# Kernel tuning notes

Measured on AMD Instinct MI355X. Metric: run time of the kernel, lower is better.

## Reference

```python
import jax, jax.numpy as jnp
from jax import lax
import numpy as np

EPS = 1e-5

def lc2d(x, w, b, stride):
    # x: [B,H,W]; w: [oh,ow,kh,kw] unshared kernels; b: [oh,ow]
    oh, ow, kh, kw = w.shape
    hi = jnp.arange(oh)[:, None] * stride + jnp.arange(kh)[None, :]  # [oh,kh]
    wi = jnp.arange(ow)[:, None] * stride + jnp.arange(kw)[None, :]  # [ow,kw]
    patches = x[:, hi[:, None, :, None], wi[None, :, None, :]]  # [B,oh,ow,kh,kw]
    return jnp.einsum('bhwkl,hwkl->bhw', patches, w) + b

def ln2d(x, g, b):
    # LayerNorm over last two dims (per-sample)
    m = jnp.mean(x, axis=(-2, -1), keepdims=True)
    v = jnp.var(x, axis=(-2, -1), keepdims=True)
    return (x - m) * lax.rsqrt(v + EPS) * g + b

def maxpool2(x):
    # MaxPool2d(kernel=2, stride=2) on [B,H,W]
    return lax.reduce_window(x, -jnp.inf, lax.max, (1, 2, 2), (1, 2, 2), 'VALID')

def setup_inputs() -> dict:
    key = jax.random.key(0)
    ks = iter(jax.random.split(key, 16))
    d = {'x': jax.random.normal(next(ks), (128, 224, 224), jnp.float32)}
    layer_specs = [(109, 7), (50, 5), (48, 3), (22, 3), (20, 3), (8, 3)]
    for i, (o, k) in enumerate(layer_specs, 1):
        std = float(np.sqrt(2.0 / (k + k)))  # xavier_normal_ on a [k,k] kernel
        d[f'w{i}'] = jax.random.normal(next(ks), (o, o, k, k), jnp.float32) * std
        d[f'b{i}'] = jnp.zeros((o, o), jnp.float32)
        d[f'g{i}'] = jnp.ones((o, o), jnp.float32)
        d[f'be{i}'] = jnp.zeros((o, o), jnp.float32)
    d['fcw'] = jax.random.normal(next(ks), (1000, 64), jnp.float32) * float(np.sqrt(1.0 / 64))
    d['fcb'] = jnp.zeros((1000,), jnp.float32)
    return d

def reference(x, w1, b1, g1, be1, w2, b2, g2, be2, w3, b3, g3, be3,
              w4, b4, g4, be4, w5, b5, g5, be5, w6, b6, g6, be6, fcw, fcb):
    # dropout is inference-mode identity (p=0)
    h = ln2d(jax.nn.relu(lc2d(x, w1, b1, 2)), g1, be1)   # [B,109,109]
    h = maxpool2(h)                                       # [B,54,54]
    h = ln2d(jax.nn.relu(lc2d(h, w2, b2, 1)), g2, be2)   # [B,50,50]
    h = ln2d(jax.nn.relu(lc2d(h, w3, b3, 1)), g3, be3)   # [B,48,48]
    h = maxpool2(h)                                       # [B,24,24]
    h = ln2d(jax.nn.relu(lc2d(h, w4, b4, 1)), g4, be4)   # [B,22,22]
    h = ln2d(jax.nn.relu(lc2d(h, w5, b5, 1)), g5, be5)   # [B,20,20]
    h = maxpool2(h)                                       # [B,10,10]
    h = ln2d(jax.nn.relu(lc2d(h, w6, b6, 1)), g6, be6)   # [B,8,8]
    logits = h.reshape(h.shape[0], -1) @ fcw.T + fcb      # [B,1000]
    return jax.nn.softmax(logits, axis=1)
```

## Files before the change

kernel.cpp:

```cpp
#include <hip/hip_runtime.h>
#include <math.h>

static constexpr float kEps = 1e-5f;

__global__ __launch_bounds__(256)
void transpose_w1(const float* __restrict__ w1, float* __restrict__ t1)
{
    const int tid = blockIdx.x * blockDim.x + threadIdx.x;
    const int nt  = gridDim.x * blockDim.x;
    for (int i = tid; i < 49 * 109 * 112; i += nt) {
        const int kk = i / (109 * 112), r = i % (109 * 112);
        const int oh = r / 112, ow = r % 112;
        t1[i] = (ow < 109) ? w1[(oh * 109 + ow) * 49 + kk] : 0.f;
    }
}

__global__ __launch_bounds__(128)
void conv1(const float* __restrict__ x, const float* __restrict__ wt,
           const float* __restrict__ bias, float* __restrict__ y,
           float* __restrict__ partial,
           const float* __restrict__ w2, const float* __restrict__ w3,
           const float* __restrict__ w4, const float* __restrict__ w5,
           const float* __restrict__ w6,
           const float* __restrict__ g1, const float* __restrict__ be1,
           float* __restrict__ w2t, float* __restrict__ w3t,
           float* __restrict__ w4t, float* __restrict__ w5t,
           float* __restrict__ w6t,
           float4* __restrict__ g1p, float4* __restrict__ be1p)
{
    constexpr int IN = 224, OUT = 109, K = 7, RPS = 4, QPR = 28, NS = 28;
    constexpr int ROWS = (RPS - 1) * 2 + K;
    __shared__ __align__(16) float xs0[ROWS * IN];
    __shared__ __align__(16) float xs1[ROWS * IN];
    __shared__ float red[2][4];

    const int s = blockIdx.x, bp = blockIdx.y, t = threadIdx.x;

    if (bp == 64) {
        const int tid = s * 128 + t;
        const int nt  = 28 * 128;
        for (int i = tid; i < 25 * 50 * 52; i += nt) {
            const int kk = i / (50 * 52), r = i % (50 * 52);
            const int oh = r / 52, ow = r % 52;
            w2t[i] = (ow < 50) ? w2[(oh * 50 + ow) * 25 + kk] : 0.f;
        }
        for (int i = tid; i < 9 * 2304; i += nt) {
            const int kk = i / 2304, idx = i % 2304;
            w3t[i] = w3[idx * 9 + kk];
        }
        for (int i = tid; i < 9 * 22 * 24; i += nt) {
            const int kk = i / (22 * 24), r = i % (22 * 24);
            const int oh = r / 24, ow = r % 24;
            w4t[i] = (ow < 22) ? w4[(oh * 22 + ow) * 9 + kk] : 0.f;
        }
        for (int i = tid; i < 9 * 400; i += nt) {
            const int kk = i / 400, idx = i % 400;
            w5t[i] = w5[idx * 9 + kk];
        }
        for (int i = tid; i < 9 * 64; i += nt) {
            const int kk = i / 64, idx = i % 64;
            w6t[i] = w6[idx * 9 + kk];
        }
        for (int i = tid; i < 54 * 54; i += nt) {
            const int ph = i / 54, pw = i - ph * 54;
            const int i00 = (2 * ph) * 109 + 2 * pw, i10 = i00 + 109;
            g1p[i]  = make_float4(g1[i00],  g1[i00 + 1],  g1[i10],  g1[i10 + 1]);
            be1p[i] = make_float4(be1[i00], be1[i00 + 1], be1[i10], be1[i10 + 1]);
        }
        return;
    }

    const int b0 = 2 * bp, b1 = b0 + 1;
    const int oh0 = s * RPS, ih0 = oh0 * 2;
    const int nrows = min(ROWS, IN - ih0);
    {
        const float4* g0 = (const float4*)(x + ((size_t)b0 * IN + ih0) * IN);
        const float4* g1r = (const float4*)(x + ((size_t)b1 * IN + ih0) * IN);
        float4* s0 = (float4*)xs0;
        float4* s1 = (float4*)xs1;
        const int n4 = nrows * (IN / 4);
        for (int i = t; i < n4; i += 128) { s0[i] = g0[i]; s1[i] = g1r[i]; }
    }
    __syncthreads();

    float lsum0 = 0.f, lsq0 = 0.f, lsum1 = 0.f, lsq1 = 0.f;
    if (t < RPS * QPR) {
        const int r = t / QPR, qc = t - r * QPR;
        const int oh = oh0 + r, ow0 = qc * 4;
        if (oh < OUT) {
            float acc0[4], acc1[4];
            #pragma unroll
            for (int o = 0; o < 4; ++o) {
                const float bv = (ow0 + o < OUT) ? bias[oh * OUT + ow0 + o] : 0.f;
                acc0[o] = bv; acc1[o] = bv;
            }
            const int lr0 = r * 2, c0 = ow0 * 2;
            #pragma unroll
            for (int kh = 0; kh < K; ++kh) {
                const float* p0 = xs0 + (lr0 + kh) * IN + c0;
                const float* p1 = xs1 + (lr0 + kh) * IN + c0;
                float a0[14], a1[14];
                #pragma unroll
                for (int i = 0; i < 7; ++i) {
                    const float2 v0 = *(const float2*)(p0 + 2 * i);
                    const float2 v1 = *(const float2*)(p1 + 2 * i);
                    a0[2 * i] = v0.x; a0[2 * i + 1] = v0.y;
                    a1[2 * i] = v1.x; a1[2 * i + 1] = v1.y;
                }
                #pragma unroll
                for (int kw = 0; kw < K; ++kw) {
                    const float4 w4 = *(const float4*)(wt + ((size_t)(kh * 7 + kw) * OUT + oh) * 112 + ow0);
                    acc0[0] = fmaf(a0[kw    ], w4.x, acc0[0]);  acc1[0] = fmaf(a1[kw    ], w4.x, acc1[0]);
                    acc0[1] = fmaf(a0[kw + 2], w4.y, acc0[1]);  acc1[1] = fmaf(a1[kw + 2], w4.y, acc1[1]);
                    acc0[2] = fmaf(a0[kw + 4], w4.z, acc0[2]);  acc1[2] = fmaf(a1[kw + 4], w4.z, acc1[2]);
                    acc0[3] = fmaf(a0[kw + 6], w4.w, acc0[3]);  acc1[3] = fmaf(a1[kw + 6], w4.w, acc1[3]);
                }
            }
            float4 st0, st1;
            #pragma unroll
            for (int o = 0; o < 4; ++o) {
                const float v0 = fmaxf(acc0[o], 0.f), v1 = fmaxf(acc1[o], 0.f);
                if (ow0 + o < OUT) {
                    lsum0 += v0; lsq0 = fmaf(v0, v0, lsq0);
                    lsum1 += v1; lsq1 = fmaf(v1, v1, lsq1);
                }
                (&st0.x)[o] = v0; (&st1.x)[o] = v1;
            }
            *(float4*)(y + ((size_t)b0 * OUT + oh) * 112 + ow0) = st0;
            *(float4*)(y + ((size_t)b1 * OUT + oh) * 112 + ow0) = st1;
        }
    }
    #pragma unroll
    for (int off = 32; off > 0; off >>= 1) {
        lsum0 += __shfl_down(lsum0, off, 64);  lsq0 += __shfl_down(lsq0, off, 64);
        lsum1 += __shfl_down(lsum1, off, 64);  lsq1 += __shfl_down(lsq1, off, 64);
    }
    if ((t & 63) == 0) {
        const int w = t >> 6;
        red[w][0] = lsum0; red[w][1] = lsq0; red[w][2] = lsum1; red[w][3] = lsq1;
    }
    __syncthreads();
    if (t == 0) {
        const float a = red[0][0] + red[1][0], bq = red[0][1] + red[1][1];
        const float c = red[0][2] + red[1][2], d  = red[0][3] + red[1][3];
        partial[((size_t)b0 * NS + s) * 2]     = a;
        partial[((size_t)b0 * NS + s) * 2 + 1] = bq;
        partial[((size_t)b1 * NS + s) * 2]     = c;
        partial[((size_t)b1 * NS + s) * 2 + 1] = d;
    }
}

__device__ inline float2 bstats(float ls, float lq, float invN, float (*red)[2], int t)
{
    #pragma unroll
    for (int off = 32; off > 0; off >>= 1) {
        ls += __shfl_down(ls, off, 64);
        lq += __shfl_down(lq, off, 64);
    }
    if ((t & 63) == 0) { red[t >> 6][0] = ls; red[t >> 6][1] = lq; }
    __syncthreads();
    float s = 0.f, q = 0.f;
    #pragma unroll
    for (int w = 0; w < 16; ++w) { s += red[w][0]; q += red[w][1]; }
    const float m = s * invN;
    return make_float2(m, rsqrtf(q * invN - m * m + kEps));
}

__global__ __launch_bounds__(1024)
void tail(const float* __restrict__ y1, const float* __restrict__ partial,
          const float4* __restrict__ g1p, const float4* __restrict__ be1p,
          const float* __restrict__ w2t, const float* __restrict__ b2,
          const float* __restrict__ g2, const float* __restrict__ be2,
          const float* __restrict__ w3t, const float* __restrict__ b3,
          const float* __restrict__ g3, const float* __restrict__ be3,
          const float* __restrict__ w4t, const float* __restrict__ b4,
          const float* __restrict__ g4, const float* __restrict__ be4,
          const float* __restrict__ w5t, const float* __restrict__ b5,
          const float* __restrict__ g5, const float* __restrict__ be5,
          const float* __restrict__ w6t, const float* __restrict__ b6,
          const float* __restrict__ g6, const float* __restrict__ be6,
          const float* __restrict__ fcw, const float* __restrict__ fcb,
          float* __restrict__ out)
{
    __shared__ __align__(16) float xs54[54 * 54 + 8];
    __shared__ __align__(16) float y50[50 * 52];
    __shared__ __align__(16) float y48[48 * 48];
    __shared__ __align__(16) float xs24[24 * 24 + 8];
    __shared__ __align__(16) float y22[22 * 24];
    __shared__ __align__(16) float y20[20 * 20];
    __shared__ __align__(16) float xs10[100];
    __shared__ float y8[64], h[64];
    __shared__ float red[16][2];

    const int b = blockIdx.x, t = threadIdx.x;
    const int lane = t & 63;

    float s = 0.f, q = 0.f;
    if (lane < 28) {
        const float2 p = *(const float2*)(partial + ((size_t)b * 28 + lane) * 2);
        s = p.x; q = p.y;
    }
    #pragma unroll
    for (int off = 32; off > 0; off >>= 1) {
        s += __shfl_down(s, off, 64);
        q += __shfl_down(q, off, 64);
    }
    s = __shfl(s, 0, 64); q = __shfl(q, 0, 64);
    const float m1 = s / 11881.f;
    const float r1 = rsqrtf(q / 11881.f - m1 * m1 + kEps);

    const float* yb = y1 + (size_t)b * 109 * 112;
    #pragma unroll
    for (int it = 0; it < 3; ++it) {
        const int idx = t + it * 1024;
        if (idx < 54 * 54) {
            const int ph = idx / 54, pw = idx - ph * 54;
            const int r0 = 2 * ph, c0 = 2 * pw;
            const float2 u0 = *(const float2*)(yb + r0 * 112 + c0);
            const float2 u1 = *(const float2*)(yb + (r0 + 1) * 112 + c0);
            const float4 g = g1p[idx], be = be1p[idx];
            const float v0 = (u0.x - m1) * r1 * g.x + be.x;
            const float v1 = (u0.y - m1) * r1 * g.y + be.y;
            const float v2 = (u1.x - m1) * r1 * g.z + be.z;
            const float v3 = (u1.y - m1) * r1 * g.w + be.w;
            xs54[ph * 54 + pw] = fmaxf(fmaxf(v0, v1), fmaxf(v2, v3));
        }
    }
    __syncthreads();

    float ls = 0.f, lq = 0.f;
    if (t < 650) {
        const int oh = t / 13, qc = t - oh * 13;
        const int ow0 = qc * 4;
        float acc[4];
        #pragma unroll
        for (int o = 0; o < 4; ++o) acc[o] = (ow0 + o < 50) ? b2[oh * 50 + ow0 + o] : 0.f;
        #pragma unroll
        for (int kh = 0; kh < 5; ++kh) {
            const float* xp = xs54 + (oh + kh) * 54 + ow0;
            float a[8];
            #pragma unroll
            for (int i = 0; i < 4; ++i) {
                const float2 v = *(const float2*)(xp + 2 * i);
                a[2 * i] = v.x; a[2 * i + 1] = v.y;
            }
            #pragma unroll
            for (int kw = 0; kw < 5; ++kw) {
                const float4 w4 = *(const float4*)(w2t + ((size_t)(kh * 5 + kw) * 50 + oh) * 52 + ow0);
                acc[0] = fmaf(a[kw    ], w4.x, acc[0]);
                acc[1] = fmaf(a[kw + 1], w4.y, acc[1]);
                acc[2] = fmaf(a[kw + 2], w4.z, acc[2]);
                acc[3] = fmaf(a[kw + 3], w4.w, acc[3]);
            }
        }
        #pragma unroll
        for (int o = 0; o < 4; ++o) {
            const float v = fmaxf(acc[o], 0.f);
            y50[oh * 52 + ow0 + o] = v;
            if (ow0 + o < 50) { ls += v; lq = fmaf(v, v, lq); }
        }
    }
    const float2 s2 = bstats(ls, lq, 1.f / 2500.f, red, t);

    #pragma unroll
    for (int it = 0; it < 3; ++it) {
        const int idx = t + it * 1024;
        if (idx < 2500) {
            const int oh = idx / 50, ow = idx - oh * 50;
            const int p = oh * 52 + ow;
            y50[p] = (y50[p] - s2.x) * s2.y * g2[idx] + be2[idx];
        }
    }
    __syncthreads();

    ls = 0.f; lq = 0.f;
    if (t < 576) {
        const int oh = t / 12, qc = t - oh * 12;
        const int ow0 = qc * 4;
        float acc[4];
        #pragma unroll
        for (int o = 0; o < 4; ++o) acc[o] = b3[oh * 48 + ow0 + o];
        #pragma unroll
        for (int kh = 0; kh < 3; ++kh) {
            const float* xp = y50 + (oh + kh) * 52 + ow0;
            float a[6];
            #pragma unroll
            for (int i = 0; i < 3; ++i) {
                const float2 v = *(const float2*)(xp + 2 * i);
                a[2 * i] = v.x; a[2 * i + 1] = v.y;
            }
            #pragma unroll
            for (int kw = 0; kw < 3; ++kw) {
                const float4 w4 = *(const float4*)(w3t + (size_t)(kh * 3 + kw) * 2304 + oh * 48 + ow0);
                acc[0] = fmaf(a[kw    ], w4.x, acc[0]);
                acc[1] = fmaf(a[kw + 1], w4.y, acc[1]);
                acc[2] = fmaf(a[kw + 2], w4.z, acc[2]);
                acc[3] = fmaf(a[kw + 3], w4.w, acc[3]);
            }
        }
        float4 st;
        #pragma unroll
        for (int o = 0; o < 4; ++o) {
            const float v = fmaxf(acc[o], 0.f);
            (&st.x)[o] = v; ls += v; lq = fmaf(v, v, lq);
        }
        *(float4*)(y48 + oh * 48 + ow0) = st;
    }
    const float2 s3 = bstats(ls, lq, 1.f / 2304.f, red, t);

    if (t < 576) {
        const int ph = t / 24, pw = t - ph * 24;
        const int r0 = 2 * ph, c0 = 2 * pw;
        const float2 u0 = *(const float2*)(y48 + r0 * 48 + c0);
        const float2 u1 = *(const float2*)(y48 + (r0 + 1) * 48 + c0);
        const int i00 = r0 * 48 + c0, i10 = i00 + 48;
        const float v0 = (u0.x - s3.x) * s3.y * g3[i00]     + be3[i00];
        const float v1 = (u0.y - s3.x) * s3.y * g3[i00 + 1] + be3[i00 + 1];
        const float v2 = (u1.x - s3.x) * s3.y * g3[i10]     + be3[i10];
        const float v3 = (u1.y - s3.x) * s3.y * g3[i10 + 1] + be3[i10 + 1];
        xs24[ph * 24 + pw] = fmaxf(fmaxf(v0, v1), fmaxf(v2, v3));
    }
    __syncthreads();

    ls = 0.f; lq = 0.f;
    if (t < 132) {
        const int oh = t / 6, qc = t - oh * 6;
        const int ow0 = qc * 4;
        float acc[4];
        #pragma unroll
        for (int o = 0; o < 4; ++o) acc[o] = (ow0 + o < 22) ? b4[oh * 22 + ow0 + o] : 0.f;
        #pragma unroll
        for (int kh = 0; kh < 3; ++kh) {
            const float* xp = xs24 + (oh + kh) * 24 + ow0;
            float a[6];
            #pragma unroll
            for (int i = 0; i < 3; ++i) {
                const float2 v = *(const float2*)(xp + 2 * i);
                a[2 * i] = v.x; a[2 * i + 1] = v.y;
            }
            #pragma unroll
            for (int kw = 0; kw < 3; ++kw) {
                const float4 w4 = *(const float4*)(w4t + ((size_t)(kh * 3 + kw) * 22 + oh) * 24 + ow0);
                acc[0] = fmaf(a[kw    ], w4.x, acc[0]);
                acc[1] = fmaf(a[kw + 1], w4.y, acc[1]);
                acc[2] = fmaf(a[kw + 2], w4.z, acc[2]);
                acc[3] = fmaf(a[kw + 3], w4.w, acc[3]);
            }
        }
        #pragma unroll
        for (int o = 0; o < 4; ++o) {
            const float v = fmaxf(acc[o], 0.f);
            y22[oh * 24 + ow0 + o] = v;
            if (ow0 + o < 22) { ls += v; lq = fmaf(v, v, lq); }
        }
    }
    const float2 s4 = bstats(ls, lq, 1.f / 484.f, red, t);

    if (t < 484) {
        const int oh = t / 22, ow = t - oh * 22;
        const int p = oh * 24 + ow;
        y22[p] = (y22[p] - s4.x) * s4.y * g4[t] + be4[t];
    }
    __syncthreads();

    ls = 0.f; lq = 0.f;
    if (t < 100) {
        const int oh = t / 5, qc = t - oh * 5;
        const int ow0 = qc * 4;
        float acc[4];
        #pragma unroll
        for (int o = 0; o < 4; ++o) acc[o] = b5[oh * 20 + ow0 + o];
        #pragma unroll
        for (int kh = 0; kh < 3; ++kh) {
            const float* xp = y22 + (oh + kh) * 24 + ow0;
            float a[6];
            #pragma unroll
            for (int i = 0; i < 3; ++i) {
                const float2 v = *(const float2*)(xp + 2 * i);
                a[2 * i] = v.x; a[2 * i + 1] = v.y;
            }
            #pragma unroll
            for (int kw = 0; kw < 3; ++kw) {
                const float4 w4 = *(const float4*)(w5t + (size_t)(kh * 3 + kw) * 400 + oh * 20 + ow0);
                acc[0] = fmaf(a[kw    ], w4.x, acc[0]);
                acc[1] = fmaf(a[kw + 1], w4.y, acc[1]);
                acc[2] = fmaf(a[kw + 2], w4.z, acc[2]);
                acc[3] = fmaf(a[kw + 3], w4.w, acc[3]);
            }
        }
        #pragma unroll
        for (int o = 0; o < 4; ++o) {
            const float v = fmaxf(acc[o], 0.f);
            y20[oh * 20 + ow0 + o] = v;
            ls += v; lq = fmaf(v, v, lq);
        }
    }
    const float2 s5 = bstats(ls, lq, 1.f / 400.f, red, t);

    if (t < 100) {
        const int ph = t / 10, pw = t - ph * 10;
        const int r0 = 2 * ph, c0 = 2 * pw;
        const float2 u0 = *(const float2*)(y20 + r0 * 20 + c0);
        const float2 u1 = *(const float2*)(y20 + (r0 + 1) * 20 + c0);
        const int i00 = r0 * 20 + c0, i10 = i00 + 20;
        const float v0 = (u0.x - s5.x) * s5.y * g5[i00]     + be5[i00];
        const float v1 = (u0.y - s5.x) * s5.y * g5[i00 + 1] + be5[i00 + 1];
        const float v2 = (u1.x - s5.x) * s5.y * g5[i10]     + be5[i10];
        const float v3 = (u1.y - s5.x) * s5.y * g5[i10 + 1] + be5[i10 + 1];
        xs10[ph * 10 + pw] = fmaxf(fmaxf(v0, v1), fmaxf(v2, v3));
    }
    __syncthreads();

    ls = 0.f; lq = 0.f;
    if (t < 16) {
        const int oh = t / 2, qc = t - oh * 2;
        const int ow0 = qc * 4;
        float acc[4];
        #pragma unroll
        for (int o = 0; o < 4; ++o) acc[o] = b6[oh * 8 + ow0 + o];
        #pragma unroll
        for (int kh = 0; kh < 3; ++kh) {
            const float* xp = xs10 + (oh + kh) * 10 + ow0;
            float a[6];
            #pragma unroll
            for (int i = 0; i < 3; ++i) {
                const float2 v = *(const float2*)(xp + 2 * i);
                a[2 * i] = v.x; a[2 * i + 1] = v.y;
            }
            #pragma unroll
            for (int kw = 0; kw < 3; ++kw) {
                const float4 w4 = *(const float4*)(w6t + (size_t)(kh * 3 + kw) * 64 + oh * 8 + ow0);
                acc[0] = fmaf(a[kw    ], w4.x, acc[0]);
                acc[1] = fmaf(a[kw + 1], w4.y, acc[1]);
                acc[2] = fmaf(a[kw + 2], w4.z, acc[2]);
                acc[3] = fmaf(a[kw + 3], w4.w, acc[3]);
            }
        }
        #pragma unroll
        for (int o = 0; o < 4; ++o) {
            const float v = fmaxf(acc[o], 0.f);
            y8[oh * 8 + ow0 + o] = v;
            ls += v; lq = fmaf(v, v, lq);
        }
    }
    const float2 s6 = bstats(ls, lq, 1.f / 64.f, red, t);

    if (t < 64) h[t] = (y8[t] - s6.x) * s6.y * g6[t] + be6[t];
    __syncthreads();

    float lj = -INFINITY;
    if (t < 1000) {
        const float4* wr = (const float4*)(fcw + (size_t)t * 64);
        float acc = fcb[t];
        #pragma unroll
        for (int k = 0; k < 16; ++k) {
            const float4 w4 = wr[k];
            acc = fmaf(h[4 * k], w4.x,
                  fmaf(h[4 * k + 1], w4.y,
                  fmaf(h[4 * k + 2], w4.z,
                  fmaf(h[4 * k + 3], w4.w, acc))));
        }
        lj = acc;
    }
    float mx = lj;
    #pragma unroll
    for (int off = 32; off > 0; off >>= 1) mx = fmaxf(mx, __shfl_down(mx, off, 64));
    if (lane == 0) red[t >> 6][0] = mx;
    __syncthreads();
    float gmax = red[0][0];
    #pragma unroll
    for (int w = 1; w < 16; ++w) gmax = fmaxf(gmax, red[w][0]);

    const float e = (t < 1000) ? __expf(lj - gmax) : 0.f;
    float ssum = e;
    #pragma unroll
    for (int off = 32; off > 0; off >>= 1) ssum += __shfl_down(ssum, off, 64);
    if (lane == 0) red[t >> 6][1] = ssum;
    __syncthreads();
    float tot = 0.f;
    #pragma unroll
    for (int w = 0; w < 16; ++w) tot += red[w][1];
    if (t < 1000) out[(size_t)b * 1000 + t] = e / tot;
}

extern "C" void kernel_launch(void* const* d_in, const int* in_sizes, int n_in,
                              void* d_out, int out_size, void* d_ws, size_t ws_size,
                              hipStream_t stream) {
    const float* x   = (const float*)d_in[0];
    const float* w1  = (const float*)d_in[1];
    const float* b1  = (const float*)d_in[2];
    const float* g1  = (const float*)d_in[3];
    const float* be1 = (const float*)d_in[4];
    const float* w2  = (const float*)d_in[5];
    const float* b2  = (const float*)d_in[6];
    const float* g2  = (const float*)d_in[7];
    const float* be2 = (const float*)d_in[8];
    const float* w3  = (const float*)d_in[9];
    const float* b3  = (const float*)d_in[10];
    const float* g3  = (const float*)d_in[11];
    const float* be3 = (const float*)d_in[12];
    const float* w4  = (const float*)d_in[13];
    const float* b4  = (const float*)d_in[14];
    const float* g4  = (const float*)d_in[15];
    const float* be4 = (const float*)d_in[16];
    const float* w5  = (const float*)d_in[17];
    const float* b5  = (const float*)d_in[18];
    const float* g5  = (const float*)d_in[19];
    const float* be5 = (const float*)d_in[20];
    const float* w6  = (const float*)d_in[21];
    const float* b6  = (const float*)d_in[22];
    const float* g6  = (const float*)d_in[23];
    const float* be6 = (const float*)d_in[24];
    const float* fcw = (const float*)d_in[25];
    const float* fcb = (const float*)d_in[26];

    float* y1p  = (float*)d_ws;
    float* w1t  = y1p  + 1562624;
    float* w2t  = w1t  + 598192;
    float* w3t  = w2t  + 65000;
    float* w4t  = w3t  + 20736;
    float* w5t  = w4t  + 4752;
    float* w6t  = w5t  + 3600;
    float* part = w6t  + 576;
    float* g1pp = part + 7168;
    float* be1pp= g1pp + 11664;

    transpose_w1<<<512, 256, 0, stream>>>(w1, w1t);

    conv1<<<dim3(28, 65), 128, 0, stream>>>(x, w1t, b1, y1p, part,
                                            w2, w3, w4, w5, w6, g1, be1,
                                            w2t, w3t, w4t, w5t, w6t,
                                            (float4*)g1pp, (float4*)be1pp);

    tail<<<128, 1024, 0, stream>>>(y1p, part,
                                   (const float4*)g1pp, (const float4*)be1pp,
                                   w2t, b2, g2, be2,
                                   w3t, b3, g3, be3,
                                   w4t, b4, g4, be4,
                                   w5t, b5, g5, be5,
                                   w6t, b6, g6, be6,
                                   fcw, fcb, (float*)d_out);
}
```

Before: 53.06 us.

## Restructure conv1 with strided column mapping, padded smem rows, larger row tiles

Conv1 now assigns each thread output columns qc, qc+28, qc+56 and qc+84 instead of four adjacent columns, and w1 is transposed into a matching interleaved layout so one float4 load still fetches all four weights. Shared-memory rows are padded to a 228-float stride to spread LDS bank accesses. Each block now covers 7 output rows with 256 threads instead of 4 rows with 128, so there are 16 row strips per sample instead of 28 and less halo is reloaded. In exchange the output stores become scalar instead of float4, and each thread makes more separate LDS reads.

After: 86.16 us. +62.4%, slower.

```diff
diff --git a/kernel.cpp b/kernel.cpp
--- a/kernel.cpp
+++ b/kernel.cpp
@@ -9,13 +9,16 @@
     const int tid = blockIdx.x * blockDim.x + threadIdx.x;
     const int nt  = gridDim.x * blockDim.x;
     for (int i = tid; i < 49 * 109 * 112; i += nt) {
-        const int kk = i / (109 * 112), r = i % (109 * 112);
-        const int oh = r / 112, ow = r % 112;
-        t1[i] = (ow < 109) ? w1[(oh * 109 + ow) * 49 + kk] : 0.f;
+        const int kk = i / 12208;
+        const int rem = i - kk * 12208;
+        const int oh = rem / 112, ow = rem - oh * 112;
+        const int qc = ow % 28, o = ow / 28;
+        const float v = (ow < 109) ? w1[(oh * 109 + ow) * 49 + kk] : 0.f;
+        t1[(((size_t)kk * 109 + oh) * 28 + qc) * 4 + o] = v;
     }
 }
 
-__global__ __launch_bounds__(128)
+__global__ __launch_bounds__(256)
 void conv1(const float* __restrict__ x, const float* __restrict__ wt,
            const float* __restrict__ bias, float* __restrict__ y,
            float* __restrict__ partial,
@@ -28,17 +31,18 @@
            float* __restrict__ w6t,
            float4* __restrict__ g1p, float4* __restrict__ be1p)
 {
-    constexpr int IN = 224, OUT = 109, K = 7, RPS = 4, QPR = 28, NS = 28;
-    constexpr int ROWS = (RPS - 1) * 2 + K;
-    __shared__ __align__(16) float xs0[ROWS * IN];
-    __shared__ __align__(16) float xs1[ROWS * IN];
-    __shared__ float red[2][4];
+    constexpr int IN = 224, OUT = 109, RPS = 7, NS = 16;
+    constexpr int ROWS = (RPS - 1) * 2 + 7;
+    constexpr int RSTR = 228;
+    __shared__ __align__(16) float xs0[ROWS * RSTR + 12];
+    __shared__ __align__(16) float xs1[ROWS * RSTR + 12];
+    __shared__ float red[4][4];
 
     const int s = blockIdx.x, bp = blockIdx.y, t = threadIdx.x;
 
     if (bp == 64) {
-        const int tid = s * 128 + t;
-        const int nt  = 28 * 128;
+        const int tid = s * 256 + t;
+        const int nt  = 16 * 256;
         for (int i = tid; i < 25 * 50 * 52; i += nt) {
             const int kk = i / (50 * 52), r = i % (50 * 52);
             const int oh = r / 52, ow = r % 52;
@@ -76,58 +80,70 @@
     {
         const float4* g0 = (const float4*)(x + ((size_t)b0 * IN + ih0) * IN);
         const float4* g1r = (const float4*)(x + ((size_t)b1 * IN + ih0) * IN);
-        float4* s0 = (float4*)xs0;
-        float4* s1 = (float4*)xs1;
-        const int n4 = nrows * (IN / 4);
-        for (int i = t; i < n4; i += 128) { s0[i] = g0[i]; s1[i] = g1r[i]; }
+        const int n4 = nrows * 56;
+        for (int i = t; i < n4; i += 256) {
+            const int row = i / 56, j = i - row * 56;
+            *(float4*)(xs0 + row * RSTR + 4 * j) = g0[row * 56 + j];
+            *(float4*)(xs1 + row * RSTR + 4 * j) = g1r[row * 56 + j];
+        }
     }
     __syncthreads();
 
     float lsum0 = 0.f, lsq0 = 0.f, lsum1 = 0.f, lsq1 = 0.f;
-    if (t < RPS * QPR) {
-        const int r = t / QPR, qc = t - r * QPR;
-        const int oh = oh0 + r, ow0 = qc * 4;
+    if (t < RPS * 28) {
+        const int r = t / 28, qc = t - r * 28;
+        const int oh = oh0 + r;
         if (oh < OUT) {
+            const float4* wv = (const float4*)wt;
             float acc0[4], acc1[4];
             #pragma unroll
             for (int o = 0; o < 4; ++o) {
-                const float bv = (ow0 + o < OUT) ? bias[oh * OUT + ow0 + o] : 0.f;
+                const int ow = qc + 28 * o;
+                const float bv = (ow < OUT) ? bias[oh * OUT + ow] : 0.f;
                 acc0[o] = bv; acc1[o] = bv;
             }
-            const int lr0 = r * 2, c0 = ow0 * 2;
-            #pragma unroll
-            for (int kh = 0; kh < K; ++kh) {
-                const float* p0 = xs0 + (lr0 + kh) * IN + c0;
-                const float* p1 = xs1 + (lr0 + kh) * IN + c0;
-                float a0[14], a1[14];
+            #pragma unroll
+            for (int kh = 0; kh < 7; ++kh) {
+                float4 w[7];
                 #pragma unroll
-                for (int i = 0; i < 7; ++i) {
-                    const float2 v0 = *(const float2*)(p0 + 2 * i);
-                    const float2 v1 = *(const float2*)(p1 + 2 * i);
-                    a0[2 * i] = v0.x; a0[2 * i + 1] = v0.y;
-                    a1[2 * i] = v1.x; a1[2 * i + 1] = v1.y;
+                for (int kw = 0; kw < 7; ++kw)
+                    w[kw] = wv[(((size_t)(kh * 7 + kw) * OUT) + oh) * 28 + qc];
+                const int ro = (2 * r + kh) * RSTR;
+                #pragma unroll
+                for (int o = 0; o < 4; ++o) {
+                    int cb = 2 * qc + 56 * o;
+                    if (o == 3) cb = min(cb, 216);
+                    const float* p0 = xs0 + ro + cb;
+                    const float* p1 = xs1 + ro + cb;
+                    float a0[8], a1[8];
+                    #pragma unroll
+                    for (int i2 = 0; i2 < 4; ++i2) {
+                        const float2 v0 = *(const float2*)(p0 + 2 * i2);
+                        const float2 v1 = *(const float2*)(p1 + 2 * i2);
+                        a0[2 * i2] = v0.x; a0[2 * i2 + 1] = v0.y;
+                        a1[2 * i2] = v1.x; a1[2 * i2 + 1] = v1.y;
+                    }
+                    #pragma unroll
+                    for (int kw = 0; kw < 7; ++kw) {
+                        const float wvv = (&w[kw].x)[o];
+                        acc0[o] = fmaf(a0[kw], wvv, acc0[o]);
+                        acc1[o] = fmaf(a1[kw], wvv, acc1[o]);
+                    }
                 }
-                #pragma unroll
-                for (int kw = 0; kw < K; ++kw) {
-                    const float4 w4 = *(const float4*)(wt + ((size_t)(kh * 7 + kw) * OUT + oh) * 112 + ow0);
-                    acc0[0] = fmaf(a0[kw    ], w4.x, acc0[0]);  acc1[0] = fmaf(a1[kw    ], w4.x, acc1[0]);
-                    acc0[1] = fmaf(a0[kw + 2], w4.y, acc0[1]);  acc1[1] = fmaf(a1[kw + 2], w4.y, acc1[1]);
-                    acc0[2] = fmaf(a0[kw + 4], w4.z, acc0[2]);  acc1[2] = fmaf(a1[kw + 4], w4.z, acc1[2]);
-                    acc0[3] = fmaf(a0[kw + 6], w4.w, acc0[3]);  acc1[3] = fmaf(a1[kw + 6], w4.w, acc1[3]);
-                }
-            }
-            float4 st0, st1;
+            }
+            float* yb0 = y + ((size_t)b0 * OUT + oh) * 112;
+            float* yb1 = y + ((size_t)b1 * OUT + oh) * 112;
             #pragma unroll
             for (int o = 0; o < 4; ++o) {
-                const float v0 = fmaxf(acc0[o], 0.f), v1 = fmaxf(acc1[o], 0.f);
-                if (ow0 + o < OUT) {
+                const int ow = qc + 28 * o;
+                if (ow < OUT) {
+                    const float v0 = fmaxf(acc0[o], 0.f);
+                    const float v1 = fmaxf(acc1[o], 0.f);
+                    yb0[ow] = v0; yb1[ow] = v1;
                     lsum0 += v0; lsq0 = fmaf(v0, v0, lsq0);
                     lsum1 += v1; lsq1 = fmaf(v1, v1, lsq1);
                 }
-                (&st0.x)[o] = v0; (&st1.x)[o] = v1;
-            }
-            *(float4*)(y + ((size_t)b0 * OUT + oh) * 112 + ow0) = st0;
-            *(float4*)(y + ((size_t)b1 * OUT + oh) * 112 + ow0) = st1;
+            }
         }
     }
     #pragma unroll
@@ -141,8 +157,9 @@
     }
     __syncthreads();
     if (t == 0) {
-        const float a = red[0][0] + red[1][0], bq = red[0][1] + red[1][1];
-        const float c = red[0][2] + red[1][2], d  = red[0][3] + red[1][3];
+        float a = 0, bq = 0, c = 0, d = 0;
+        #pragma unroll
+        for (int w = 0; w < 4; ++w) { a += red[w][0]; bq += red[w][1]; c += red[w][2]; d += red[w][3]; }
         partial[((size_t)b0 * NS + s) * 2]     = a;
         partial[((size_t)b0 * NS + s) * 2 + 1] = bq;
         partial[((size_t)b1 * NS + s) * 2]     = c;
@@ -196,8 +213,8 @@
     const int lane = t & 63;
 
     float s = 0.f, q = 0.f;
-    if (lane < 28) {
-        const float2 p = *(const float2*)(partial + ((size_t)b * 28 + lane) * 2);
+    if (lane < 16) {
+        const float2 p = *(const float2*)(partial + ((size_t)b * 16 + lane) * 2);
         s = p.x; q = p.y;
     }
     #pragma unroll
@@ -522,12 +539,12 @@
     float* w5t  = w4t  + 4752;
     float* w6t  = w5t  + 3600;
     float* part = w6t  + 576;
-    float* g1pp = part + 7168;
+    float* g1pp = part + 4096;
     float* be1pp= g1pp + 11664;
 
     transpose_w1<<<512, 256, 0, stream>>>(w1, w1t);
 
-    conv1<<<dim3(28, 65), 128, 0, stream>>>(x, w1t, b1, y1p, part,
+    conv1<<<dim3(16, 65), 256, 0, stream>>>(x, w1t, b1, y1p, part,
                                             w2, w3, w4, w5, w6, g1, be1,
                                             w2t, w3t, w4t, w5t, w6t,
                                             (float4*)g1pp, (float4*)be1pp);
```

## Retile conv1 with deinterleaved shared rows, larger strips, and tile the w1 transpose

Applied to the files above, without the earlier changes.

conv1 now gives each block 8 output rows instead of 4, using 448 threads that each compute 2 adjacent outputs for two samples. The input rows are stored in shared memory split into even and odd columns, so the stride-2 taps read contiguous data. This cuts the halo rows reloaded per output row and the per-thread register footprint, at the cost of a larger shared-memory footprint per block and fewer blocks. transpose_w1 now stages 64 kernels in shared memory so global reads are coalesced. It no longer writes the zero padding columns of the transposed weights. The partial-statistics buffer and the tail's reduction shrink to 14 strips to match.

After: 67.73 us. 1.28x slower.

```diff
diff --git a/kernel.cpp b/kernel.cpp
--- a/kernel.cpp
+++ b/kernel.cpp
@@ -6,16 +6,23 @@
 __global__ __launch_bounds__(256)
 void transpose_w1(const float* __restrict__ w1, float* __restrict__ t1)
 {
-    const int tid = blockIdx.x * blockDim.x + threadIdx.x;
-    const int nt  = gridDim.x * blockDim.x;
-    for (int i = tid; i < 49 * 109 * 112; i += nt) {
-        const int kk = i / (109 * 112), r = i % (109 * 112);
-        const int oh = r / 112, ow = r % 112;
-        t1[i] = (ow < 109) ? w1[(oh * 109 + ow) * 49 + kk] : 0.f;
+    __shared__ float ws[64 * 49];
+    const int b = blockIdx.x, t = threadIdx.x;
+    const int base = b * 64;
+    const int n = min(64, 11881 - base);
+    for (int i = t; i < n * 49; i += 256) ws[i] = w1[(size_t)base * 49 + i];
+    __syncthreads();
+    for (int i = t; i < 49 * 64; i += 256) {
+        const int kk = i >> 6, l = i & 63;
+        if (l < n) {
+            const int idx = base + l;
+            const int oh = idx / 109, ow = idx - 109 * oh;
+            t1[((size_t)kk * 109 + oh) * 112 + ow] = ws[l * 49 + kk];
+        }
     }
 }
 
-__global__ __launch_bounds__(128)
+__global__ __launch_bounds__(448)
 void conv1(const float* __restrict__ x, const float* __restrict__ wt,
            const float* __restrict__ bias, float* __restrict__ y,
            float* __restrict__ partial,
@@ -28,17 +35,18 @@
            float* __restrict__ w6t,
            float4* __restrict__ g1p, float4* __restrict__ be1p)
 {
-    constexpr int IN = 224, OUT = 109, K = 7, RPS = 4, QPR = 28, NS = 28;
-    constexpr int ROWS = (RPS - 1) * 2 + K;
-    __shared__ __align__(16) float xs0[ROWS * IN];
-    __shared__ __align__(16) float xs1[ROWS * IN];
-    __shared__ float red[2][4];
+    constexpr int IN = 224, OUT = 109, RPS = 8, NSTR = 14;
+    constexpr int ROWS = (RPS - 1) * 2 + 7;
+    constexpr int HW = 114;
+    __shared__ __align__(8) float xe[2 * ROWS * HW];
+    __shared__ __align__(8) float xo[2 * ROWS * HW];
+    __shared__ float red[7][4];
 
     const int s = blockIdx.x, bp = blockIdx.y, t = threadIdx.x;
 
     if (bp == 64) {
-        const int tid = s * 128 + t;
-        const int nt  = 28 * 128;
+        const int tid = s * 448 + t;
+        const int nt  = 14 * 448;
         for (int i = tid; i < 25 * 50 * 52; i += nt) {
             const int kk = i / (50 * 52), r = i % (50 * 52);
             const int oh = r / 52, ow = r % 52;
@@ -73,80 +81,95 @@
     const int b0 = 2 * bp, b1 = b0 + 1;
     const int oh0 = s * RPS, ih0 = oh0 * 2;
     const int nrows = min(ROWS, IN - ih0);
+
     {
-        const float4* g0 = (const float4*)(x + ((size_t)b0 * IN + ih0) * IN);
-        const float4* g1r = (const float4*)(x + ((size_t)b1 * IN + ih0) * IN);
-        float4* s0 = (float4*)xs0;
-        float4* s1 = (float4*)xs1;
-        const int n4 = nrows * (IN / 4);
-        for (int i = t; i < n4; i += 128) { s0[i] = g0[i]; s1[i] = g1r[i]; }
-    }
-    __syncthreads();
-
-    float lsum0 = 0.f, lsq0 = 0.f, lsum1 = 0.f, lsq1 = 0.f;
-    if (t < RPS * QPR) {
-        const int r = t / QPR, qc = t - r * QPR;
-        const int oh = oh0 + r, ow0 = qc * 4;
-        if (oh < OUT) {
-            float acc0[4], acc1[4];
-            #pragma unroll
-            for (int o = 0; o < 4; ++o) {
-                const float bv = (ow0 + o < OUT) ? bias[oh * OUT + ow0 + o] : 0.f;
-                acc0[o] = bv; acc1[o] = bv;
-            }
-            const int lr0 = r * 2, c0 = ow0 * 2;
-            #pragma unroll
-            for (int kh = 0; kh < K; ++kh) {
-                const float* p0 = xs0 + (lr0 + kh) * IN + c0;
-                const float* p1 = xs1 + (lr0 + kh) * IN + c0;
-                float a0[14], a1[14];
+        const int n4 = nrows * 56;
+        for (int i = t; i < 2 * n4; i += 448) {
+            const int smp = (i < n4) ? 0 : 1;
+            const int rem = i - smp * n4;
+            const int row = rem / 56, j = rem - row * 56;
+            const int bb = smp ? b1 : b0;
+            const float4 v = *(const float4*)(x + ((size_t)bb * IN + ih0 + row) * IN + 4 * j);
+            const int o = (smp * ROWS + row) * HW + 2 * j;
+            *(float2*)(xe + o) = make_float2(v.x, v.z);
+            *(float2*)(xo + o) = make_float2(v.y, v.w);
+        }
+    }
+    __syncthreads();
+
+    float ls0 = 0.f, lq0 = 0.f, ls1 = 0.f, lq1 = 0.f;
+    {
+        const int r = t / 56, qc = t - r * 56;
+        const int oh = oh0 + r;
+        if (oh < OUT && qc < 55) {
+            const bool valid1 = (2 * qc + 1 < OUT);
+            float acc00 = bias[oh * OUT + 2 * qc];
+            float acc01 = valid1 ? bias[oh * OUT + 2 * qc + 1] : 0.f;
+            float acc10 = acc00, acc11 = acc01;
+            #pragma unroll
+            for (int kh = 0; kh < 7; ++kh) {
+                const int lr = 2 * r + kh;
+                const int off0 = lr * HW + 2 * qc;
+                const int off1 = (ROWS + lr) * HW + 2 * qc;
+                float e0[5], o0[4], e1[5], o1[4];
+                { const float2 u = *(const float2*)(xe + off0);     e0[0]=u.x; e0[1]=u.y; }
+                { const float2 u = *(const float2*)(xe + off0 + 2); e0[2]=u.x; e0[3]=u.y; }
+                e0[4] = xe[off0 + 4];
+                { const float2 u = *(const float2*)(xo + off0);     o0[0]=u.x; o0[1]=u.y; }
+                { const float2 u = *(const float2*)(xo + off0 + 2); o0[2]=u.x; o0[3]=u.y; }
+                { const float2 u = *(const float2*)(xe + off1);     e1[0]=u.x; e1[1]=u.y; }
+                { const float2 u = *(const float2*)(xe + off1 + 2); e1[2]=u.x; e1[3]=u.y; }
+                e1[4] = xe[off1 + 4];
+                { const float2 u = *(const float2*)(xo + off1);     o1[0]=u.x; o1[1]=u.y; }
+                { const float2 u = *(const float2*)(xo + off1 + 2); o1[2]=u.x; o1[3]=u.y; }
                 #pragma unroll
-                for (int i = 0; i < 7; ++i) {
-                    const float2 v0 = *(const float2*)(p0 + 2 * i);
-                    const float2 v1 = *(const float2*)(p1 + 2 * i);
-                    a0[2 * i] = v0.x; a0[2 * i + 1] = v0.y;
-                    a1[2 * i] = v1.x; a1[2 * i + 1] = v1.y;
+                for (int kw = 0; kw < 7; ++kw) {
+                    const float2 w2v = *(const float2*)(wt + ((size_t)(kh * 7 + kw) * OUT + oh) * 112 + 2 * qc);
+                    const int hi = kw >> 1;
+                    const float xa0 = (kw & 1) ? o0[hi] : e0[hi];
+                    const float xb0 = (kw & 1) ? o0[hi + 1] : e0[hi + 1];
+                    const float xa1 = (kw & 1) ? o1[hi] : e1[hi];
+                    const float xb1 = (kw & 1) ? o1[hi + 1] : e1[hi + 1];
+                    acc00 = fmaf(xa0, w2v.x, acc00);
+                    acc01 = fmaf(xb0, w2v.y, acc01);
+                    acc10 = fmaf(xa1, w2v.x, acc10);
+                    acc11 = fmaf(xb1, w2v.y, acc11);
                 }
-                #pragma unroll
-                for (int kw = 0; kw < K; ++kw) {
-                    const float4 w4 = *(const float4*)(wt + ((size_t)(kh * 7 + kw) * OUT + oh) * 112 + ow0);
-                    acc0[0] = fmaf(a0[kw    ], w4.x, acc0[0]);  acc1[0] = fmaf(a1[kw    ], w4.x, acc1[0]);
-                    acc0[1] = fmaf(a0[kw + 2], w4.y, acc0[1]);  acc1[1] = fmaf(a1[kw + 2], w4.y, acc1[1]);
-                    acc0[2] = fmaf(a0[kw + 4], w4.z, acc0[2]);  acc1[2] = fmaf(a1[kw + 4], w4.z, acc1[2]);
-                    acc0[3] = fmaf(a0[kw + 6], w4.w, acc0[3]);  acc1[3] = fmaf(a1[kw + 6], w4.w, acc1[3]);
-                }
-            }
-            float4 st0, st1;
-            #pragma unroll
-            for (int o = 0; o < 4; ++o) {
-                const float v0 = fmaxf(acc0[o], 0.f), v1 = fmaxf(acc1[o], 0.f);
-                if (ow0 + o < OUT) {
-                    lsum0 += v0; lsq0 = fmaf(v0, v0, lsq0);
-                    lsum1 += v1; lsq1 = fmaf(v1, v1, lsq1);
-                }
-                (&st0.x)[o] = v0; (&st1.x)[o] = v1;
-            }
-            *(float4*)(y + ((size_t)b0 * OUT + oh) * 112 + ow0) = st0;
-            *(float4*)(y + ((size_t)b1 * OUT + oh) * 112 + ow0) = st1;
+            }
+            const float v00 = fmaxf(acc00, 0.f), v01 = fmaxf(acc01, 0.f);
+            const float v10 = fmaxf(acc10, 0.f), v11 = fmaxf(acc11, 0.f);
+            float* r0 = y + ((size_t)b0 * OUT + oh) * 112 + 2 * qc;
+            float* r1 = y + ((size_t)b1 * OUT + oh) * 112 + 2 * qc;
+            if (valid1) {
+                *(float2*)r0 = make_float2(v00, v01);
+                *(float2*)r1 = make_float2(v10, v11);
+                ls0 += v00 + v01; lq0 = fmaf(v00, v00, fmaf(v01, v01, lq0));
+                ls1 += v10 + v11; lq1 = fmaf(v10, v10, fmaf(v11, v11, lq1));
+            } else {
+                r0[0] = v00; r1[0] = v10;
+                ls0 += v00; lq0 = fmaf(v00, v00, lq0);
+                ls1 += v10; lq1 = fmaf(v10, v10, lq1);
+            }
         }
     }
     #pragma unroll
     for (int off = 32; off > 0; off >>= 1) {
-        lsum0 += __shfl_down(lsum0, off, 64);  lsq0 += __shfl_down(lsq0, off, 64);
-        lsum1 += __shfl_down(lsum1, off, 64);  lsq1 += __shfl_down(lsq1, off, 64);
+        ls0 += __shfl_down(ls0, off, 64);  lq0 += __shfl_down(lq0, off, 64);
+        ls1 += __shfl_down(ls1, off, 64);  lq1 += __shfl_down(lq1, off, 64);
     }
     if ((t & 63) == 0) {
         const int w = t >> 6;
-        red[w][0] = lsum0; red[w][1] = lsq0; red[w][2] = lsum1; red[w][3] = lsq1;
+        red[w][0] = ls0; red[w][1] = lq0; red[w][2] = ls1; red[w][3] = lq1;
     }
     __syncthreads();
     if (t == 0) {
-        const float a = red[0][0] + red[1][0], bq = red[0][1] + red[1][1];
-        const float c = red[0][2] + red[1][2], d  = red[0][3] + red[1][3];
-        partial[((size_t)b0 * NS + s) * 2]     = a;
-        partial[((size_t)b0 * NS + s) * 2 + 1] = bq;
-        partial[((size_t)b1 * NS + s) * 2]     = c;
-        partial[((size_t)b1 * NS + s) * 2 + 1] = d;
+        float a = 0, bq = 0, c = 0, d = 0;
+        #pragma unroll
+        for (int w = 0; w < 7; ++w) { a += red[w][0]; bq += red[w][1]; c += red[w][2]; d += red[w][3]; }
+        partial[((size_t)b0 * NSTR + s) * 2]     = a;
+        partial[((size_t)b0 * NSTR + s) * 2 + 1] = bq;
+        partial[((size_t)b1 * NSTR + s) * 2]     = c;
+        partial[((size_t)b1 * NSTR + s) * 2 + 1] = d;
     }
 }
 
@@ -196,8 +219,8 @@
     const int lane = t & 63;
 
     float s = 0.f, q = 0.f;
-    if (lane < 28) {
-        const float2 p = *(const float2*)(partial + ((size_t)b * 28 + lane) * 2);
+    if (lane < 14) {
+        const float2 p = *(const float2*)(partial + ((size_t)b * 14 + lane) * 2);
         s = p.x; q = p.y;
     }
     #pragma unroll
@@ -522,12 +545,12 @@
     float* w5t  = w4t  + 4752;
     float* w6t  = w5t  + 3600;
     float* part = w6t  + 576;
-    float* g1pp = part + 7168;
+    float* g1pp = part + 3584;
     float* be1pp= g1pp + 11664;
 
-    transpose_w1<<<512, 256, 0, stream>>>(w1, w1t);
-
-    conv1<<<dim3(28, 65), 128, 0, stream>>>(x, w1t, b1, y1p, part,
+    transpose_w1<<<186, 256, 0, stream>>>(w1, w1t);
+
+    conv1<<<dim3(14, 65), 448, 0, stream>>>(x, w1t, b1, y1p, part,
                                             w2, w3, w4, w5, w6, g1, be1,
                                             w2t, w3t, w4t, w5t, w6t,
                                             (float4*)g1pp, (float4*)be1pp);
```

## Transpose input to sample-minor layout and map batch across lanes in conv1

Applied to the files above, without the earlier changes.

Replaces the weight-transpose kernel and row-tiled conv1 with a kernel that transposes the input x into a [pos][sample] layout. The new conv1 puts one sample per lane and reads each output position's weights as wave-uniform values via readfirstlane. This removes the w1 transpose and the per-lane weight loads, and per-row LN partials are written for the tail kernel to reduce. In exchange it adds a full 25 MB read-write transpose of x. It also uses a small 218-block grid with uncoalesced strided stores of y.

Result: slower. 64.65 us (+21.9%).

```diff
diff --git a/kernel.cpp b/kernel.cpp
--- a/kernel.cpp
+++ b/kernel.cpp
@@ -4,21 +4,7 @@
 static constexpr float kEps = 1e-5f;
 
 __global__ __launch_bounds__(256)
-void transpose_w1(const float* __restrict__ w1, float* __restrict__ t1)
-{
-    const int tid = blockIdx.x * blockDim.x + threadIdx.x;
-    const int nt  = gridDim.x * blockDim.x;
-    for (int i = tid; i < 49 * 109 * 112; i += nt) {
-        const int kk = i / (109 * 112), r = i % (109 * 112);
-        const int oh = r / 112, ow = r % 112;
-        t1[i] = (ow < 109) ? w1[(oh * 109 + ow) * 49 + kk] : 0.f;
-    }
-}
-
-__global__ __launch_bounds__(128)
-void conv1(const float* __restrict__ x, const float* __restrict__ wt,
-           const float* __restrict__ bias, float* __restrict__ y,
-           float* __restrict__ partial,
+void xpose(const float* __restrict__ x, float* __restrict__ xt,
            const float* __restrict__ w2, const float* __restrict__ w3,
            const float* __restrict__ w4, const float* __restrict__ w5,
            const float* __restrict__ w6,
@@ -28,17 +14,10 @@
            float* __restrict__ w6t,
            float4* __restrict__ g1p, float4* __restrict__ be1p)
 {
-    constexpr int IN = 224, OUT = 109, K = 7, RPS = 4, QPR = 28, NS = 28;
-    constexpr int ROWS = (RPS - 1) * 2 + K;
-    __shared__ __align__(16) float xs0[ROWS * IN];
-    __shared__ __align__(16) float xs1[ROWS * IN];
-    __shared__ float red[2][4];
-
-    const int s = blockIdx.x, bp = blockIdx.y, t = threadIdx.x;
-
-    if (bp == 64) {
-        const int tid = s * 128 + t;
-        const int nt  = 28 * 128;
+    const int bid = blockIdx.x, t = threadIdx.x;
+    if (bid >= 784) {
+        const int tid = (bid - 784) * 256 + t;
+        const int nt  = 14 * 256;
         for (int i = tid; i < 25 * 50 * 52; i += nt) {
             const int kk = i / (50 * 52), r = i % (50 * 52);
             const int oh = r / 52, ow = r % 52;
@@ -70,83 +49,68 @@
         return;
     }
 
-    const int b0 = 2 * bp, b1 = b0 + 1;
-    const int oh0 = s * RPS, ih0 = oh0 * 2;
-    const int nrows = min(ROWS, IN - ih0);
-    {
-        const float4* g0 = (const float4*)(x + ((size_t)b0 * IN + ih0) * IN);
-        const float4* g1r = (const float4*)(x + ((size_t)b1 * IN + ih0) * IN);
-        float4* s0 = (float4*)xs0;
-        float4* s1 = (float4*)xs1;
-        const int n4 = nrows * (IN / 4);
-        for (int i = t; i < n4; i += 128) { s0[i] = g0[i]; s1[i] = g1r[i]; }
-    }
-    __syncthreads();
-
-    float lsum0 = 0.f, lsq0 = 0.f, lsum1 = 0.f, lsq1 = 0.f;
-    if (t < RPS * QPR) {
-        const int r = t / QPR, qc = t - r * QPR;
-        const int oh = oh0 + r, ow0 = qc * 4;
-        if (oh < OUT) {
-            float acc0[4], acc1[4];
-            #pragma unroll
-            for (int o = 0; o < 4; ++o) {
-                const float bv = (ow0 + o < OUT) ? bias[oh * OUT + ow0 + o] : 0.f;
-                acc0[o] = bv; acc1[o] = bv;
-            }
-            const int lr0 = r * 2, c0 = ow0 * 2;
-            #pragma unroll
-            for (int kh = 0; kh < K; ++kh) {
-                const float* p0 = xs0 + (lr0 + kh) * IN + c0;
-                const float* p1 = xs1 + (lr0 + kh) * IN + c0;
-                float a0[14], a1[14];
+    __shared__ float ls[64 * 133];
+    const int pos0 = bid * 64;
+    for (int i = t; i < 8192; i += 256) {
+        const int s = i >> 6, j = i & 63;
+        ls[j * 133 + s] = x[(size_t)s * 50176 + pos0 + j];
+    }
+    __syncthreads();
+    for (int i = t; i < 8192; i += 256) {
+        const int j = i >> 7, s = i & 127;
+        xt[(size_t)(pos0 + j) * 128 + s] = ls[j * 133 + s];
+    }
+}
+
+__global__ __launch_bounds__(512)
+void conv1(const float* __restrict__ xt, const float* __restrict__ w1,
+           const float* __restrict__ bias, float* __restrict__ y,
+           float* __restrict__ partial)
+{
+    __shared__ float redS[8][64], redQ[8][64];
+    const int oh = blockIdx.x;
+    const int grp = blockIdx.y;
+    const int t = threadIdx.x;
+    const int w = t >> 6, lane = t & 63;
+    const int smp = grp * 64 + lane;
+
+    float lsum = 0.f, lsq = 0.f;
+    for (int ch = w; ch < 28; ch += 8) {
+        const int ow0 = ch * 4;
+        float xv[7][13];
+        const size_t base = ((size_t)(2 * oh) * 224 + 2 * ow0) * 128 + smp;
+        #pragma unroll
+        for (int r = 0; r < 7; ++r) {
+            #pragma unroll
+            for (int c = 0; c < 13; ++c)
+                xv[r][c] = xt[base + ((size_t)(r * 224 + c)) * 128];
+        }
+        #pragma unroll
+        for (int o = 0; o < 4; ++o) {
+            const int ow = ow0 + o;
+            if (ow < 109) {
+                const int idx = __builtin_amdgcn_readfirstlane(oh * 109 + ow);
+                const float* __restrict__ wr = w1 + (size_t)idx * 49;
+                float acc = bias[idx];
                 #pragma unroll
-                for (int i = 0; i < 7; ++i) {
-                    const float2 v0 = *(const float2*)(p0 + 2 * i);
-                    const float2 v1 = *(const float2*)(p1 + 2 * i);
-                    a0[2 * i] = v0.x; a0[2 * i + 1] = v0.y;
-                    a1[2 * i] = v1.x; a1[2 * i + 1] = v1.y;
+                for (int kh = 0; kh < 7; ++kh) {
+                    #pragma unroll
+                    for (int kw = 0; kw < 7; ++kw)
+                        acc = fmaf(xv[kh][2 * o + kw], wr[kh * 7 + kw], acc);
                 }
-                #pragma unroll
-                for (int kw = 0; kw < K; ++kw) {
-                    const float4 w4 = *(const float4*)(wt + ((size_t)(kh * 7 + kw) * OUT + oh) * 112 + ow0);
-                    acc0[0] = fmaf(a0[kw    ], w4.x, acc0[0]);  acc1[0] = fmaf(a1[kw    ], w4.x, acc1[0]);
-                    acc0[1] = fmaf(a0[kw + 2], w4.y, acc0[1]);  acc1[1] = fmaf(a1[kw + 2], w4.y, acc1[1]);
-                    acc0[2] = fmaf(a0[kw + 4], w4.z, acc0[2]);  acc1[2] = fmaf(a1[kw + 4], w4.z, acc1[2]);
-                    acc0[3] = fmaf(a0[kw + 6], w4.w, acc0[3]);  acc1[3] = fmaf(a1[kw + 6], w4.w, acc1[3]);
-                }
-            }
-            float4 st0, st1;
-            #pragma unroll
-            for (int o = 0; o < 4; ++o) {
-                const float v0 = fmaxf(acc0[o], 0.f), v1 = fmaxf(acc1[o], 0.f);
-                if (ow0 + o < OUT) {
-                    lsum0 += v0; lsq0 = fmaf(v0, v0, lsq0);
-                    lsum1 += v1; lsq1 = fmaf(v1, v1, lsq1);
-                }
-                (&st0.x)[o] = v0; (&st1.x)[o] = v1;
-            }
-            *(float4*)(y + ((size_t)b0 * OUT + oh) * 112 + ow0) = st0;
-            *(float4*)(y + ((size_t)b1 * OUT + oh) * 112 + ow0) = st1;
-        }
-    }
-    #pragma unroll
-    for (int off = 32; off > 0; off >>= 1) {
-        lsum0 += __shfl_down(lsum0, off, 64);  lsq0 += __shfl_down(lsq0, off, 64);
-        lsum1 += __shfl_down(lsum1, off, 64);  lsq1 += __shfl_down(lsq1, off, 64);
-    }
-    if ((t & 63) == 0) {
-        const int w = t >> 6;
-        red[w][0] = lsum0; red[w][1] = lsq0; red[w][2] = lsum1; red[w][3] = lsq1;
-    }
-    __syncthreads();
-    if (t == 0) {
-        const float a = red[0][0] + red[1][0], bq = red[0][1] + red[1][1];
-        const float c = red[0][2] + red[1][2], d  = red[0][3] + red[1][3];
-        partial[((size_t)b0 * NS + s) * 2]     = a;
-        partial[((size_t)b0 * NS + s) * 2 + 1] = bq;
-        partial[((size_t)b1 * NS + s) * 2]     = c;
-        partial[((size_t)b1 * NS + s) * 2 + 1] = d;
+                const float v = fmaxf(acc, 0.f);
+                y[((size_t)smp * 109 + oh) * 112 + ow] = v;
+                lsum += v; lsq = fmaf(v, v, lsq);
+            }
+        }
+    }
+    redS[w][lane] = lsum; redQ[w][lane] = lsq;
+    __syncthreads();
+    if (w == 0) {
+        float s = 0.f, q = 0.f;
+        #pragma unroll
+        for (int i = 0; i < 8; ++i) { s += redS[i][lane]; q += redQ[i][lane]; }
+        *(float2*)(partial + ((size_t)smp * 109 + oh) * 2) = make_float2(s, q);
     }
 }
 
@@ -195,10 +159,14 @@
     const int b = blockIdx.x, t = threadIdx.x;
     const int lane = t & 63;
 
-    float s = 0.f, q = 0.f;
-    if (lane < 28) {
-        const float2 p = *(const float2*)(partial + ((size_t)b * 28 + lane) * 2);
+    float s, q;
+    {
+        const float2 p = *(const float2*)(partial + ((size_t)b * 109 + lane) * 2);
         s = p.x; q = p.y;
+        if (lane < 45) {
+            const float2 p2 = *(const float2*)(partial + ((size_t)b * 109 + 64 + lane) * 2);
+            s += p2.x; q += p2.y;
+        }
     }
     #pragma unroll
     for (int off = 32; off > 0; off >>= 1) {
@@ -514,23 +482,23 @@
     const float* fcw = (const float*)d_in[25];
     const float* fcb = (const float*)d_in[26];
 
-    float* y1p  = (float*)d_ws;
-    float* w1t  = y1p  + 1562624;
-    float* w2t  = w1t  + 598192;
+    float* xt   = (float*)d_ws;
+    float* y1p  = xt   + 6422528;
+    float* w2t  = y1p  + 1562624;
     float* w3t  = w2t  + 65000;
     float* w4t  = w3t  + 20736;
     float* w5t  = w4t  + 4752;
     float* w6t  = w5t  + 3600;
     float* part = w6t  + 576;
-    float* g1pp = part + 7168;
+    float* g1pp = part + 27904;
     float* be1pp= g1pp + 11664;
 
-    transpose_w1<<<512, 256, 0, stream>>>(w1, w1t);
-
-    conv1<<<dim3(28, 65), 128, 0, stream>>>(x, w1t, b1, y1p, part,
-                                            w2, w3, w4, w5, w6, g1, be1,
-                                            w2t, w3t, w4t, w5t, w6t,
-                                            (float4*)g1pp, (float4*)be1pp);
+    xpose<<<798, 256, 0, stream>>>(x, xt,
+                                   w2, w3, w4, w5, w6, g1, be1,
+                                   w2t, w3t, w4t, w5t, w6t,
+                                   (float4*)g1pp, (float4*)be1pp);
+
+    conv1<<<dim3(109, 2), 512, 0, stream>>>(xt, w1, b1, y1p, part);
 
     tail<<<128, 1024, 0, stream>>>(y1p, part,
                                    (const float4*)g1pp, (const float4*)be1pp,
```
